# Kernel optimization log

Measured on AMD Instinct MI355X. Metric: run time of the kernel, lower is better.

## Reference

```python
import jax, jax.numpy as jnp
import numpy as np

EPS = 1e-12  # matches F.normalize default eps
TEMPERATURE = 1.0  # normlized=False -> temperature reset to 1.0
W1, W3 = 1.0, 0.3
LAMBDA1, LAMBDA2 = 1.0, 1.0


def setup_inputs() -> dict:
    key = jax.random.key(0)
    kq, kp = jax.random.split(key)
    q_hidden = jax.random.normal(kq, (16, 64, 768), dtype=jnp.float32)
    p_hidden = jax.random.normal(kp, (128, 256, 768), dtype=jnp.float32)
    return {"q_hidden": q_hidden, "p_hidden": p_hidden}


def _l2norm(x):
    n = jnp.linalg.norm(x, axis=-1, keepdims=True)
    return x / jnp.maximum(n, EPS)


def _ce(scores, target):
    # nn.CrossEntropyLoss(reduction='mean')
    ls = jax.nn.log_softmax(scores, axis=-1)
    return -jnp.mean(ls[jnp.arange(scores.shape[0]), target])


def _kld_log_target_batchmean(inp_log, tgt_log):
    # nn.KLDivLoss(reduction='batchmean', log_target=True)
    return jnp.sum(jnp.exp(tgt_log) * (tgt_log - inp_log)) / inp_log.shape[0]


def reference(q_hidden, p_hidden):
    # cls pooling (normlized=False -> no normalize of pooled reps)
    q_reps = q_hidden[:, 0]  # [Bq, D]
    p_reps = p_hidden[:, 0]  # [Bp, D]

    # multivector maxsim over normalized token embeddings
    qn = _l2norm(q_hidden)  # [Bq, Lq, D]
    pn = _l2norm(p_hidden)  # [Bp, Lp, D]
    sim = jnp.einsum('qid,pjd->qpij', qn, pn)  # [Bq, Bp, Lq, Lp]
    mv_scores = jnp.max(jnp.max(sim, axis=-1), axis=-1)  # [Bq, Bp]

    # in-batch-negative contrastive path (training)
    scores = jnp.matmul(q_reps, p_reps.T) / TEMPERATURE  # [Bq, Bp]
    mv_scores = mv_scores / TEMPERATURE
    Bq = scores.shape[0]
    group_size = p_reps.shape[0] // Bq
    target = jnp.arange(Bq) * group_size

    s_inter = W1 * scores + W3 * mv_scores
    loss_dense1 = _ce(scores, target)
    loss_mulvec1 = _ce(mv_scores, target)
    loss_inter = _ce(s_inter, target)

    s_logits1 = jax.nn.log_softmax(scores, axis=1)
    s_logits2 = jax.nn.log_softmax(mv_scores, axis=1)
    t_logits = jax.nn.log_softmax(s_inter, axis=1)
    loss_dense2 = _kld_log_target_batchmean(s_logits1, t_logits)
    # NOTE: source overwrites loss_mulvec1 with the KLD term (faithful bug reproduction)
    loss_mulvec1 = _kld_log_target_batchmean(s_logits2, t_logits)

    L1 = 0.3 * (loss_dense1 * LAMBDA1 + loss_mulvec1 * LAMBDA2 + loss_inter)
    L2 = 0.2 * (loss_dense2 * LAMBDA1 + loss_mulvec1 * LAMBDA2)
    loss = (L1 + L2) * 0.5
    return loss
```

## Files before the change

### kernel.cpp

```cpp
#include <hip/hip_runtime.h>
#include <hip/hip_bf16.h>

#define D   768
#define D2  384
#define NQ  16
#define NP  128
#define QI  64
#define PJ  256
#define MQ  (NQ*QI)
#define MP  (NP*PJ)
#define NROWBLK ((MP + MQ) / 4)

typedef __attribute__((ext_vector_type(8)))  int   int8v;
typedef __attribute__((ext_vector_type(16))) float floatx16;

#define LDS_AS __attribute__((address_space(3)))
#define GLB_AS __attribute__((address_space(1)))

static __device__ __forceinline__ void async_copy16(const uchar* g, uchar* l) {
    __builtin_amdgcn_global_load_lds((const GLB_AS uint32_t*)g,
                                     (LDS_AS uint32_t*)l, 16, 0, 0);
}

static __device__ __forceinline__ uint enc4(float4 v, float inv) {
    uint r = 0;
    const float* f = (const float*)&v;
    #pragma unroll
    for (int i = 0; i < 4; i++) {
        float x = f[i] * inv;
        float y = fabsf(x) * 16.0f;
        uint c;
        if (y < 2.25f) c = (uint)(int)rintf(y + y);
        else           c = y < 3.5f ? 5u : (y < 5.0f ? 6u : 7u);
        c |= (__float_as_uint(x) >> 28) & 8u;
        r |= c << (4 * i);
    }
    return r;
}

__global__ __launch_bounds__(256) void norm_scores(const float* __restrict__ ph,
                                                   const float* __restrict__ qh,
                                                   uchar* __restrict__ P4,
                                                   uchar* __restrict__ Q4,
                                                   float* __restrict__ scores) {
    const int wave = threadIdx.x >> 6, lane = threadIdx.x & 63;
    if (blockIdx.x < NROWBLK) {
        int row = blockIdx.x * 4 + wave;
        const float* in; uchar* out;
        if (row < MP) { in = ph; out = P4; }
        else          { in = qh; out = Q4; row -= MP; }
        const float4* r4 = (const float4*)(in + (size_t)row * D);

        float4 x0 = r4[lane], x1 = r4[lane + 64], x2 = r4[lane + 128];
        float ss = x0.x*x0.x + x0.y*x0.y + x0.z*x0.z + x0.w*x0.w
                 + x1.x*x1.x + x1.y*x1.y + x1.z*x1.z + x1.w*x1.w
                 + x2.x*x2.x + x2.y*x2.y + x2.z*x2.z + x2.w*x2.w;
        #pragma unroll
        for (int o = 32; o > 0; o >>= 1) ss += __shfl_xor(ss, o, 64);
        float inv = 1.0f / fmaxf(sqrtf(ss), 1e-12f);

        ushort* o2 = (ushort*)(out + (size_t)row * D2);
        o2[lane]       = (ushort)enc4(x0, inv);
        o2[lane + 64]  = (ushort)enc4(x1, inv);
        o2[lane + 128] = (ushort)enc4(x2, inv);
    } else {
        const int bid = (blockIdx.x - NROWBLK) * 4 + wave;
        const int q = bid >> 7, p = bid & 127;
        const float4* qr = (const float4*)(qh + (size_t)q * QI * D);
        const float4* pr = (const float4*)(ph + (size_t)p * PJ * D);
        float s = 0.f;
        #pragma unroll
        for (int k = 0; k < 3; k++) {
            float4 a = qr[lane + k * 64], b = pr[lane + k * 64];
            s += a.x * b.x + a.y * b.y + a.z * b.z + a.w * b.w;
        }
        #pragma unroll
        for (int o = 32; o > 0; o >>= 1) s += __shfl_xor(s, o, 64);
        if (lane == 0) scores[q * NP + p] = s;
    }
}

#define SCALE16 0x7B7B7B7Bu

static __device__ __forceinline__ int8v ld_frag4(const uchar* rowp, int off) {
    uint4 u = *(const uint4*)(rowp + off);
    int8v v;
    v[0] = u.x; v[1] = u.y; v[2] = u.z; v[3] = u.w;
    v[4] = 0;   v[5] = 0;   v[6] = 0;   v[7] = 0;
    return v;
}

__global__ __launch_bounds__(256, 2) void sim_max_kernel(const uchar* __restrict__ Q4,
                                                         const uchar* __restrict__ P4,
                                                         float* __restrict__ mv) {
    const int p  = blockIdx.x;
    const int qp = blockIdx.y;
    __shared__ uchar lA[128 * 128];
    __shared__ uchar lB[256 * 128];
    __shared__ float smax[4];

    const int t = threadIdx.x;
    const int wave = t >> 6, lane = t & 63;
    const int qi = wave >> 1, pj = wave & 1;

    const int lrow = lane >> 3;
    const int dmaoff = lrow * D2 + (((lane & 7) ^ lrow) << 4);

    const int r  = lane & 31;
    const int kh = lane >> 5;
    const int rx = r & 7;

    const uchar* Abase = Q4 + (size_t)(qp * 128) * D2;
    const uchar* Bbase = P4 + (size_t)p * PJ * D2;

    floatx16 acc[2][4];
    #pragma unroll
    for (int i = 0; i < 2; i++)
        #pragma unroll
        for (int j = 0; j < 4; j++)
            #pragma unroll
            for (int e = 0; e < 16; e++) acc[i][j][e] = 0.f;

    for (int k0 = 0; k0 < D2; k0 += 128) {
        __syncthreads();
        #pragma unroll
        for (int g = 0; g < 4; g++) {
            const int R0 = wave * 32 + g * 8;
            async_copy16(Abase + (size_t)R0 * D2 + k0 + dmaoff, lA + R0 * 128);
        }
        #pragma unroll
        for (int g = 0; g < 8; g++) {
            const int R0 = wave * 64 + g * 8;
            async_copy16(Bbase + (size_t)R0 * D2 + k0 + dmaoff, lB + R0 * 128);
        }
        __syncthreads();

        #pragma unroll
        for (int s = 0; s < 4; s++) {
            const int off = ((s * 2 + kh) ^ rx) << 4;
            int8v a[2];
            #pragma unroll
            for (int i = 0; i < 2; i++)
                a[i] = ld_frag4(lA + (qi * 64 + i * 32 + r) * 128, off);
            #pragma unroll
            for (int j = 0; j < 4; j++) {
                int8v b = ld_frag4(lB + (pj * 128 + j * 32 + r) * 128, off);
                #pragma unroll
                for (int i = 0; i < 2; i++)
                    acc[i][j] = __builtin_amdgcn_mfma_scale_f32_32x32x64_f8f6f4(
                        a[i], b, acc[i][j], 4, 4, 0, SCALE16, 0, SCALE16);
            }
        }
    }

    float m = -1e30f;
    #pragma unroll
    for (int i = 0; i < 2; i++)
        #pragma unroll
        for (int j = 0; j < 4; j++)
            #pragma unroll
            for (int e = 0; e < 16; e++) m = fmaxf(m, acc[i][j][e]);
    #pragma unroll
    for (int o = 32; o > 0; o >>= 1) m = fmaxf(m, __shfl_xor(m, o, 64));
    if (lane == 0) smax[wave] = m;
    __syncthreads();
    if (t < 2)
        mv[(qp * 2 + t) * NP + p] = fmaxf(smax[2 * t], smax[2 * t + 1]);
}

__global__ __launch_bounds__(64) void loss_kernel(const float* __restrict__ scores,
                                                  const float* __restrict__ mv,
                                                  float* __restrict__ out) {
    const int lane = threadIdx.x;
    float ce_s = 0.f, ce_t = 0.f, kld_s = 0.f, kld_m = 0.f;

    for (int q = 0; q < NQ; q++) {
        const float* srow = scores + q * NP;
        const float* mrow = mv + q * NP;
        float s0 = srow[lane], s1 = srow[lane + 64];
        float m0 = mrow[lane], m1 = mrow[lane + 64];
        float t0 = s0 + 0.3f * m0, t1 = s1 + 0.3f * m1;

        float xs = fmaxf(s0, s1), xm = fmaxf(m0, m1), xt = fmaxf(t0, t1);
        #pragma unroll
        for (int o = 32; o > 0; o >>= 1) {
            xs = fmaxf(xs, __shfl_xor(xs, o, 64));
            xm = fmaxf(xm, __shfl_xor(xm, o, 64));
            xt = fmaxf(xt, __shfl_xor(xt, o, 64));
        }
        float es = expf(s0 - xs) + expf(s1 - xs);
        float em = expf(m0 - xm) + expf(m1 - xm);
        float et = expf(t0 - xt) + expf(t1 - xt);
        #pragma unroll
        for (int o = 32; o > 0; o >>= 1) {
            es += __shfl_xor(es, o, 64);
            em += __shfl_xor(em, o, 64);
            et += __shfl_xor(et, o, 64);
        }
        float lse_s = xs + logf(es), lse_m = xm + logf(em), lse_t = xt + logf(et);

        float ls0 = s0 - lse_s, ls1 = s1 - lse_s;
        float lm0 = m0 - lse_m, lm1 = m1 - lse_m;
        float lt0 = t0 - lse_t, lt1 = t1 - lse_t;
        float pt0 = expf(lt0), pt1 = expf(lt1);
        kld_s += pt0 * (lt0 - ls0) + pt1 * (lt1 - ls1);
        kld_m += pt0 * (lt0 - lm0) + pt1 * (lt1 - lm1);

        const int tgt = q * (NP / NQ);
        if (lane == (tgt & 63)) {
            if (tgt < 64) { ce_s -= ls0; ce_t -= lt0; }
            else          { ce_s -= ls1; ce_t -= lt1; }
        }
    }
    #pragma unroll
    for (int o = 32; o > 0; o >>= 1) {
        ce_s  += __shfl_xor(ce_s, o, 64);
        ce_t  += __shfl_xor(ce_t, o, 64);
        kld_s += __shfl_xor(kld_s, o, 64);
        kld_m += __shfl_xor(kld_m, o, 64);
    }
    if (lane == 0) {
        ce_s /= 16.f; ce_t /= 16.f; kld_s /= 16.f; kld_m /= 16.f;
        float L1 = 0.3f * (ce_s + kld_m + ce_t);
        float L2 = 0.2f * (kld_s + kld_m);
        out[0] = 0.5f * (L1 + L2);
    }
}

extern "C" void kernel_launch(void* const* d_in, const int* in_sizes, int n_in,
                              void* d_out, int out_size, void* d_ws, size_t ws_size,
                              hipStream_t stream) {
    const float* qh = (const float*)d_in[0];
    const float* ph = (const float*)d_in[1];

    char* ws = (char*)d_ws;
    uchar* P4 = (uchar*)ws;
    uchar* Q4 = (uchar*)(ws + (size_t)MP * D2);
    float* mv = (float*)(ws + (size_t)MP * D2 + (size_t)MQ * D2);
    float* scores = mv + NQ * NP;

    norm_scores<<<NROWBLK + 512, 256, 0, stream>>>(ph, qh, P4, Q4, scores);
    sim_max_kernel<<<dim3(NP, 8), 256, 0, stream>>>(Q4, P4, mv);
    loss_kernel<<<1, 64, 0, stream>>>(scores, mv, (float*)d_out);
}
```

Baseline: 183.5 us.

## Split sim-max tile across 8 waves and parallelize loss over query rows

```diff
diff --git a/kernel.cpp b/kernel.cpp
--- a/kernel.cpp
+++ b/kernel.cpp
@@ -90,18 +90,18 @@
     return v;
 }
 
-__global__ __launch_bounds__(256, 2) void sim_max_kernel(const uchar* __restrict__ Q4,
+__global__ __launch_bounds__(512, 4) void sim_max_kernel(const uchar* __restrict__ Q4,
                                                          const uchar* __restrict__ P4,
                                                          float* __restrict__ mv) {
     const int p  = blockIdx.x;
     const int qp = blockIdx.y;
     __shared__ uchar lA[128 * 128];
     __shared__ uchar lB[256 * 128];
-    __shared__ float smax[4];
+    __shared__ float smax[8];
 
     const int t = threadIdx.x;
     const int wave = t >> 6, lane = t & 63;
-    const int qi = wave >> 1, pj = wave & 1;
+    const int qi = wave >> 2, pj = wave & 3;
 
     const int lrow = lane >> 3;
     const int dmaoff = lrow * D2 + (((lane & 7) ^ lrow) << 4);
@@ -113,24 +113,24 @@
     const uchar* Abase = Q4 + (size_t)(qp * 128) * D2;
     const uchar* Bbase = P4 + (size_t)p * PJ * D2;
 
-    floatx16 acc[2][4];
+    floatx16 acc[2][2];
     #pragma unroll
     for (int i = 0; i < 2; i++)
         #pragma unroll
-        for (int j = 0; j < 4; j++)
+        for (int j = 0; j < 2; j++)
             #pragma unroll
             for (int e = 0; e < 16; e++) acc[i][j][e] = 0.f;
 
     for (int k0 = 0; k0 < D2; k0 += 128) {
         __syncthreads();
         #pragma unroll
+        for (int g = 0; g < 2; g++) {
+            const int R0 = wave * 16 + g * 8;
+            async_copy16(Abase + (size_t)R0 * D2 + k0 + dmaoff, lA + R0 * 128);
+        }
+        #pragma unroll
         for (int g = 0; g < 4; g++) {
             const int R0 = wave * 32 + g * 8;
-            async_copy16(Abase + (size_t)R0 * D2 + k0 + dmaoff, lA + R0 * 128);
-        }
-        #pragma unroll
-        for (int g = 0; g < 8; g++) {
-            const int R0 = wave * 64 + g * 8;
             async_copy16(Bbase + (size_t)R0 * D2 + k0 + dmaoff, lB + R0 * 128);
         }
         __syncthreads();
@@ -143,8 +143,8 @@
             for (int i = 0; i < 2; i++)
                 a[i] = ld_frag4(lA + (qi * 64 + i * 32 + r) * 128, off);
             #pragma unroll
-            for (int j = 0; j < 4; j++) {
-                int8v b = ld_frag4(lB + (pj * 128 + j * 32 + r) * 128, off);
+            for (int j = 0; j < 2; j++) {
+                int8v b = ld_frag4(lB + (pj * 64 + j * 32 + r) * 128, off);
                 #pragma unroll
                 for (int i = 0; i < 2; i++)
                     acc[i][j] = __builtin_amdgcn_mfma_scale_f32_32x32x64_f8f6f4(
@@ -157,7 +157,7 @@
     #pragma unroll
     for (int i = 0; i < 2; i++)
         #pragma unroll
-        for (int j = 0; j < 4; j++)
+        for (int j = 0; j < 2; j++)
             #pragma unroll
             for (int e = 0; e < 16; e++) m = fmaxf(m, acc[i][j][e]);
     #pragma unroll
@@ -165,52 +165,52 @@
     if (lane == 0) smax[wave] = m;
     __syncthreads();
     if (t < 2)
-        mv[(qp * 2 + t) * NP + p] = fmaxf(smax[2 * t], smax[2 * t + 1]);
-}
-
-__global__ __launch_bounds__(64) void loss_kernel(const float* __restrict__ scores,
-                                                  const float* __restrict__ mv,
-                                                  float* __restrict__ out) {
-    const int lane = threadIdx.x;
-    float ce_s = 0.f, ce_t = 0.f, kld_s = 0.f, kld_m = 0.f;
-
-    for (int q = 0; q < NQ; q++) {
-        const float* srow = scores + q * NP;
-        const float* mrow = mv + q * NP;
-        float s0 = srow[lane], s1 = srow[lane + 64];
-        float m0 = mrow[lane], m1 = mrow[lane + 64];
-        float t0 = s0 + 0.3f * m0, t1 = s1 + 0.3f * m1;
-
-        float xs = fmaxf(s0, s1), xm = fmaxf(m0, m1), xt = fmaxf(t0, t1);
-        #pragma unroll
-        for (int o = 32; o > 0; o >>= 1) {
-            xs = fmaxf(xs, __shfl_xor(xs, o, 64));
-            xm = fmaxf(xm, __shfl_xor(xm, o, 64));
-            xt = fmaxf(xt, __shfl_xor(xt, o, 64));
-        }
-        float es = expf(s0 - xs) + expf(s1 - xs);
-        float em = expf(m0 - xm) + expf(m1 - xm);
-        float et = expf(t0 - xt) + expf(t1 - xt);
-        #pragma unroll
-        for (int o = 32; o > 0; o >>= 1) {
-            es += __shfl_xor(es, o, 64);
-            em += __shfl_xor(em, o, 64);
-            et += __shfl_xor(et, o, 64);
-        }
-        float lse_s = xs + logf(es), lse_m = xm + logf(em), lse_t = xt + logf(et);
-
-        float ls0 = s0 - lse_s, ls1 = s1 - lse_s;
-        float lm0 = m0 - lse_m, lm1 = m1 - lse_m;
-        float lt0 = t0 - lse_t, lt1 = t1 - lse_t;
-        float pt0 = expf(lt0), pt1 = expf(lt1);
-        kld_s += pt0 * (lt0 - ls0) + pt1 * (lt1 - ls1);
-        kld_m += pt0 * (lt0 - lm0) + pt1 * (lt1 - lm1);
-
-        const int tgt = q * (NP / NQ);
-        if (lane == (tgt & 63)) {
-            if (tgt < 64) { ce_s -= ls0; ce_t -= lt0; }
-            else          { ce_s -= ls1; ce_t -= lt1; }
-        }
+        mv[(qp * 2 + t) * NP + p] = fmaxf(fmaxf(smax[t*4], smax[t*4+1]),
+                                          fmaxf(smax[t*4+2], smax[t*4+3]));
+}
+
+__global__ __launch_bounds__(1024) void loss_kernel(const float* __restrict__ scores,
+                                                    const float* __restrict__ mv,
+                                                    float* __restrict__ out) {
+    const int q = threadIdx.x >> 6, lane = threadIdx.x & 63;
+    __shared__ float part[4][16];
+
+    const float* srow = scores + q * NP;
+    const float* mrow = mv + q * NP;
+    float s0 = srow[lane], s1 = srow[lane + 64];
+    float m0 = mrow[lane], m1 = mrow[lane + 64];
+    float t0 = s0 + 0.3f * m0, t1 = s1 + 0.3f * m1;
+
+    float xs = fmaxf(s0, s1), xm = fmaxf(m0, m1), xt = fmaxf(t0, t1);
+    #pragma unroll
+    for (int o = 32; o > 0; o >>= 1) {
+        xs = fmaxf(xs, __shfl_xor(xs, o, 64));
+        xm = fmaxf(xm, __shfl_xor(xm, o, 64));
+        xt = fmaxf(xt, __shfl_xor(xt, o, 64));
+    }
+    float es = expf(s0 - xs) + expf(s1 - xs);
+    float em = expf(m0 - xm) + expf(m1 - xm);
+    float et = expf(t0 - xt) + expf(t1 - xt);
+    #pragma unroll
+    for (int o = 32; o > 0; o >>= 1) {
+        es += __shfl_xor(es, o, 64);
+        em += __shfl_xor(em, o, 64);
+        et += __shfl_xor(et, o, 64);
+    }
+    float lse_s = xs + logf(es), lse_m = xm + logf(em), lse_t = xt + logf(et);
+
+    float ls0 = s0 - lse_s, ls1 = s1 - lse_s;
+    float lm0 = m0 - lse_m, lm1 = m1 - lse_m;
+    float lt0 = t0 - lse_t, lt1 = t1 - lse_t;
+    float pt0 = expf(lt0), pt1 = expf(lt1);
+    float kld_s = pt0 * (lt0 - ls0) + pt1 * (lt1 - ls1);
+    float kld_m = pt0 * (lt0 - lm0) + pt1 * (lt1 - lm1);
+    float ce_s = 0.f, ce_t = 0.f;
+
+    const int tgt = q * (NP / NQ);
+    if (lane == (tgt & 63)) {
+        if (tgt < 64) { ce_s = -ls0; ce_t = -lt0; }
+        else          { ce_s = -ls1; ce_t = -lt1; }
     }
     #pragma unroll
     for (int o = 32; o > 0; o >>= 1) {
@@ -220,10 +220,28 @@
         kld_m += __shfl_xor(kld_m, o, 64);
     }
     if (lane == 0) {
-        ce_s /= 16.f; ce_t /= 16.f; kld_s /= 16.f; kld_m /= 16.f;
-        float L1 = 0.3f * (ce_s + kld_m + ce_t);
-        float L2 = 0.2f * (kld_s + kld_m);
-        out[0] = 0.5f * (L1 + L2);
+        part[0][q] = ce_s; part[1][q] = ce_t;
+        part[2][q] = kld_s; part[3][q] = kld_m;
+    }
+    __syncthreads();
+    if (threadIdx.x < 64) {
+        float v0 = lane < 16 ? part[0][lane] : 0.f;
+        float v1 = lane < 16 ? part[1][lane] : 0.f;
+        float v2 = lane < 16 ? part[2][lane] : 0.f;
+        float v3 = lane < 16 ? part[3][lane] : 0.f;
+        #pragma unroll
+        for (int o = 8; o > 0; o >>= 1) {
+            v0 += __shfl_xor(v0, o, 64);
+            v1 += __shfl_xor(v1, o, 64);
+            v2 += __shfl_xor(v2, o, 64);
+            v3 += __shfl_xor(v3, o, 64);
+        }
+        if (lane == 0) {
+            v0 /= 16.f; v1 /= 16.f; v2 /= 16.f; v3 /= 16.f;
+            float L1 = 0.3f * (v0 + v3 + v1);
+            float L2 = 0.2f * (v2 + v3);
+            out[0] = 0.5f * (L1 + L2);
+        }
     }
 }
 
@@ -240,6 +258,6 @@
     float* scores = mv + NQ * NP;
 
     norm_scores<<<NROWBLK + 512, 256, 0, stream>>>(ph, qh, P4, Q4, scores);
-    sim_max_kernel<<<dim3(NP, 8), 256, 0, stream>>>(Q4, P4, mv);
-    loss_kernel<<<1, 64, 0, stream>>>(scores, mv, (float*)d_out);
-}
+    sim_max_kernel<<<dim3(NP, 8), 512, 0, stream>>>(Q4, P4, mv);
+    loss_kernel<<<1, 1024, 0, stream>>>(scores, mv, (float*)d_out);
+}
```

Result: faster. 167.2 us (-8.9%).
